# Kernel tuning notes

Hardware: AMD Instinct MI355X
Metric: run time of the kernel (lower is better)

Reference implementation:

```python
import jax, jax.numpy as jnp
import numpy as np

B, N, D = 8, 1024, 1024
E, H = 16, 4096
CAP_FACTOR = 1.25  # training-mode capacity factor
NUM_CLASSES = 345


def setup_inputs() -> dict:
    key = jax.random.key(0)
    k1, k2, k3, k4 = jax.random.split(key, 4)
    inputs = jax.random.normal(k1, (B, N, D), dtype=jnp.float32)
    current_y = jax.random.randint(k2, (B,), 0, NUM_CLASSES, dtype=jnp.int32)
    std1 = 1.0 / np.sqrt(H)  # init_ uses 1/sqrt(last dim)
    std2 = 1.0 / np.sqrt(D)
    w1 = jax.random.uniform(k3, (E, D, H), dtype=jnp.float32, minval=-std1, maxval=std1)
    w2 = jax.random.uniform(k4, (E, H, D), dtype=jnp.float32, minval=-std2, maxval=std2)
    return {"inputs": inputs, "current_y": current_y, "w1": w1, "w2": w2}


def reference(inputs, current_y, w1, w2):
    b, n, d = inputs.shape
    e = w1.shape[0]
    cap = max(min(n, int(n * CAP_FACTOR / e)), 4)  # MIN_EXPERT_CAPACITY=4
    dt = inputs.dtype

    # class-based gating: every token of sample i goes to expert y_i % e
    idx = jnp.broadcast_to(jnp.remainder(current_y, e)[:, None], (b, n))  # (b,n)
    oh = jax.nn.one_hot(idx, e, dtype=dt)                                 # (b,n,e)
    # exclusive cumsum over token dim, masked
    pos = (jnp.cumsum(oh, axis=-2) - oh) * oh                             # (b,n,e)
    mask1 = oh * (pos < cap).astype(dt)                                   # drop overflow tokens
    mask1_flat = mask1.sum(axis=-1)                                       # (b,n)
    pos_flat = pos.sum(axis=-1).astype(jnp.int32)                         # (b,n)

    # combine[b,n,e,c]; out-of-range positions -> zero row (safe_one_hot semantics)
    combine = (mask1_flat[..., None, None]
               * oh[..., None]
               * jax.nn.one_hot(pos_flat, cap, dtype=dt)[..., None, :])
    dispatch = (combine > 0).astype(dt)

    # dispatch tokens to padded expert slots: (e, b, cap, d)
    expert_in = jnp.einsum('bnd,bnec->ebcd', inputs, dispatch).reshape(e, b * cap, d)
    hidden = jax.nn.gelu(jnp.einsum('end,edh->enh', expert_in, w1), approximate=False)
    expert_out = jnp.einsum('enh,ehd->end', hidden, w2).reshape(e, b, cap, d)

    output = jnp.einsum('ebcd,bnec->bnd', expert_out, combine)
    return output
```

## Files before the change

kernel.cpp:

```cpp
#include <hip/hip_runtime.h>
#include <hip/hip_bf16.h>

#define NB   8
#define NTOK 1024
#define DDIM 1024
#define NEXP 16
#define HDIM 4096
#define CAP  80
#define BK   64
#define LDA  (BK + 8)

using bf16x8 = __attribute__((ext_vector_type(8))) __bf16;
using bf16x4 = __attribute__((ext_vector_type(4))) __bf16;
using f32x4  = __attribute__((ext_vector_type(4))) float;

__global__ __launch_bounds__(256) void moe_g1(
    const float* __restrict__ X, const int* __restrict__ Y,
    const float* __restrict__ W1, __bf16* __restrict__ Hid)
{
    const int b     = blockIdx.y;
    const int e     = Y[b] & (NEXP - 1);
    const int nbase = blockIdx.x * 64;
    const int tid   = threadIdx.x;
    const int w     = tid >> 6;
    const int l     = tid & 63;
    const int q     = l >> 4;
    const int r     = l & 15;
    const int n     = nbase + w * 16 + r;
    const int kb    = tid & 15;
    const int hb    = tid >> 4;
    const int arow  = tid >> 4;
    const int akg   = tid & 15;

    __shared__ __bf16 As[2][CAP][LDA];
    __shared__ __bf16 Bt[2][64][LDA];

    const float* Xb  = X  + (size_t)b * NTOK * DDIM;
    const float* W1e = W1 + (size_t)e * DDIM * HDIM;

    f32x4 acc[5];
    #pragma unroll
    for (int i = 0; i < 5; ++i) acc[i] = f32x4{0.f, 0.f, 0.f, 0.f};

    float4 a_reg[5];
    float4 b_reg[4];

    #pragma unroll
    for (int it = 0; it < 5; ++it)
        a_reg[it] = *(const float4*)&Xb[(size_t)(arow + 16 * it) * DDIM + akg * 4];
    #pragma unroll
    for (int kk = 0; kk < 4; ++kk)
        b_reg[kk] = *(const float4*)&W1e[(size_t)(kb * 4 + kk) * HDIM + nbase + hb * 4];

    int cur = 0;
    for (int t = 0; t < DDIM / BK; ++t) {
        #pragma unroll
        for (int it = 0; it < 5; ++it) {
            float4 v = a_reg[it];
            bf16x4 p = {(__bf16)v.x, (__bf16)v.y, (__bf16)v.z, (__bf16)v.w};
            *(bf16x4*)&As[cur][arow + 16 * it][akg * 4] = p;
        }
        {
            bf16x4 p0 = {(__bf16)b_reg[0].x, (__bf16)b_reg[1].x, (__bf16)b_reg[2].x, (__bf16)b_reg[3].x};
            bf16x4 p1 = {(__bf16)b_reg[0].y, (__bf16)b_reg[1].y, (__bf16)b_reg[2].y, (__bf16)b_reg[3].y};
            bf16x4 p2 = {(__bf16)b_reg[0].z, (__bf16)b_reg[1].z, (__bf16)b_reg[2].z, (__bf16)b_reg[3].z};
            bf16x4 p3 = {(__bf16)b_reg[0].w, (__bf16)b_reg[1].w, (__bf16)b_reg[2].w, (__bf16)b_reg[3].w};
            *(bf16x4*)&Bt[cur][hb * 4 + 0][kb * 4] = p0;
            *(bf16x4*)&Bt[cur][hb * 4 + 1][kb * 4] = p1;
            *(bf16x4*)&Bt[cur][hb * 4 + 2][kb * 4] = p2;
            *(bf16x4*)&Bt[cur][hb * 4 + 3][kb * 4] = p3;
        }
        __syncthreads();

        if (t + 1 < DDIM / BK) {
            const int k0 = (t + 1) * BK;
            #pragma unroll
            for (int it = 0; it < 5; ++it)
                a_reg[it] = *(const float4*)&Xb[(size_t)(arow + 16 * it) * DDIM + k0 + akg * 4];
            #pragma unroll
            for (int kk = 0; kk < 4; ++kk)
                b_reg[kk] = *(const float4*)&W1e[(size_t)(k0 + kb * 4 + kk) * HDIM + nbase + hb * 4];
        }

        #pragma unroll
        for (int s = 0; s < 2; ++s) {
            bf16x8 bf = *(const bf16x8*)&Bt[cur][w * 16 + r][s * 32 + q * 8];
            #pragma unroll
            for (int mt = 0; mt < 5; ++mt) {
                bf16x8 af = *(const bf16x8*)&As[cur][mt * 16 + r][s * 32 + q * 8];
                acc[mt] = __builtin_amdgcn_mfma_f32_16x16x32_bf16(af, bf, acc[mt], 0, 0, 0);
            }
        }
        cur ^= 1;
    }

    __bf16* Hb = Hid + (size_t)b * CAP * HDIM;
    #pragma unroll
    for (int mt = 0; mt < 5; ++mt)
        #pragma unroll
        for (int v = 0; v < 4; ++v) {
            int m = mt * 16 + q * 4 + v;
            float x = acc[mt][v];
            float g = 0.5f * x * (1.0f + erff(x * 0.70710678118654752f));
            Hb[(size_t)m * HDIM + n] = (__bf16)g;
        }
}

__global__ __launch_bounds__(256) void moe_g2(
    const __bf16* __restrict__ Hid, const int* __restrict__ Y,
    const float* __restrict__ W2, float* __restrict__ Out)
{
    const int b     = blockIdx.y;
    const int e     = Y[b] & (NEXP - 1);
    const int nbase = blockIdx.x * 64;
    const int kz    = blockIdx.z * (HDIM / 4);
    const int tid   = threadIdx.x;
    const int w     = tid >> 6;
    const int l     = tid & 63;
    const int q     = l >> 4;
    const int r     = l & 15;
    const int n     = nbase + w * 16 + r;
    const int kb    = tid & 15;
    const int hb    = tid >> 4;
    const int arow  = tid >> 4;
    const int akg   = tid & 15;

    __shared__ __bf16 As[2][CAP][LDA];
    __shared__ __bf16 Bt[2][64][LDA];

    const __bf16* Hb  = Hid + (size_t)b * CAP * HDIM;
    const float*  W2e = W2  + (size_t)e * HDIM * DDIM;

    f32x4 acc[5];
    #pragma unroll
    for (int i = 0; i < 5; ++i) acc[i] = f32x4{0.f, 0.f, 0.f, 0.f};

    uint2  a_reg[5];
    float4 b_reg[4];

    #pragma unroll
    for (int it = 0; it < 5; ++it)
        a_reg[it] = *(const uint2*)&Hb[(size_t)(arow + 16 * it) * HDIM + kz + akg * 4];
    #pragma unroll
    for (int kk = 0; kk < 4; ++kk)
        b_reg[kk] = *(const float4*)&W2e[(size_t)(kz + kb * 4 + kk) * DDIM + nbase + hb * 4];

    int cur = 0;
    for (int t = 0; t < (HDIM / 4) / BK; ++t) {
        #pragma unroll
        for (int it = 0; it < 5; ++it)
            *(uint2*)&As[cur][arow + 16 * it][akg * 4] = a_reg[it];
        {
            bf16x4 p0 = {(__bf16)b_reg[0].x, (__bf16)b_reg[1].x, (__bf16)b_reg[2].x, (__bf16)b_reg[3].x};
            bf16x4 p1 = {(__bf16)b_reg[0].y, (__bf16)b_reg[1].y, (__bf16)b_reg[2].y, (__bf16)b_reg[3].y};
            bf16x4 p2 = {(__bf16)b_reg[0].z, (__bf16)b_reg[1].z, (__bf16)b_reg[2].z, (__bf16)b_reg[3].z};
            bf16x4 p3 = {(__bf16)b_reg[0].w, (__bf16)b_reg[1].w, (__bf16)b_reg[2].w, (__bf16)b_reg[3].w};
            *(bf16x4*)&Bt[cur][hb * 4 + 0][kb * 4] = p0;
            *(bf16x4*)&Bt[cur][hb * 4 + 1][kb * 4] = p1;
            *(bf16x4*)&Bt[cur][hb * 4 + 2][kb * 4] = p2;
            *(bf16x4*)&Bt[cur][hb * 4 + 3][kb * 4] = p3;
        }
        __syncthreads();

        if (t + 1 < (HDIM / 4) / BK) {
            const int k0 = kz + (t + 1) * BK;
            #pragma unroll
            for (int it = 0; it < 5; ++it)
                a_reg[it] = *(const uint2*)&Hb[(size_t)(arow + 16 * it) * HDIM + k0 + akg * 4];
            #pragma unroll
            for (int kk = 0; kk < 4; ++kk)
                b_reg[kk] = *(const float4*)&W2e[(size_t)(k0 + kb * 4 + kk) * DDIM + nbase + hb * 4];
        }

        #pragma unroll
        for (int s = 0; s < 2; ++s) {
            bf16x8 bf = *(const bf16x8*)&Bt[cur][w * 16 + r][s * 32 + q * 8];
            #pragma unroll
            for (int mt = 0; mt < 5; ++mt) {
                bf16x8 af = *(const bf16x8*)&As[cur][mt * 16 + r][s * 32 + q * 8];
                acc[mt] = __builtin_amdgcn_mfma_f32_16x16x32_bf16(af, bf, acc[mt], 0, 0, 0);
            }
        }
        cur ^= 1;
    }

    float* Ob = Out + (size_t)b * NTOK * DDIM;
    #pragma unroll
    for (int mt = 0; mt < 5; ++mt)
        #pragma unroll
        for (int v = 0; v < 4; ++v) {
            int m = mt * 16 + q * 4 + v;
            atomicAdd(&Ob[(size_t)m * DDIM + n], acc[mt][v]);
        }
}

extern "C" void kernel_launch(void* const* d_in, const int* in_sizes, int n_in,
                              void* d_out, int out_size, void* d_ws, size_t ws_size,
                              hipStream_t stream) {
    const float* X  = (const float*)d_in[0];
    const int*   Y  = (const int*)d_in[1];
    const float* W1 = (const float*)d_in[2];
    const float* W2 = (const float*)d_in[3];
    float*  Out = (float*)d_out;
    __bf16* Hid = (__bf16*)d_ws;

    hipMemsetAsync(d_out, 0, (size_t)out_size * sizeof(float), stream);

    moe_g1<<<dim3(HDIM / 64, NB), 256, 0, stream>>>(X, Y, W1, Hid);
    moe_g2<<<dim3(DDIM / 64, NB, 4), 256, 0, stream>>>(Hid, Y, W2, Out);
}
```

Measured before the change: 484.3 us.

## Prepack weights and inputs to bf16 MFMA fragment layout before GEMMs

Adds pre-pass kernels that convert the first CAP rows of X to bf16 and repack each used expert's W1/W2 into a bf16 layout matching the MFMA B-fragment order. The GEMM kernels then load fragments straight from global memory, with no LDS staging, no __syncthreads and no in-loop fp32-to-bf16 conversion. The aim is to remove the shared-memory and conversion overhead in the main loops. In exchange it adds extra passes that write and re-read packed weights, and it needs about 272MB of workspace; if the workspace is smaller, the original kernels run instead.

```diff
diff --git a/kernel.cpp b/kernel.cpp
--- a/kernel.cpp
+++ b/kernel.cpp
@@ -14,44 +14,160 @@
 using bf16x4 = __attribute__((ext_vector_type(4))) __bf16;
 using f32x4  = __attribute__((ext_vector_type(4))) float;
 
+__global__ __launch_bounds__(256) void xpre(const float* __restrict__ X,
+                                            __bf16* __restrict__ Xb16)
+{
+    int idx = blockIdx.x * 256 + threadIdx.x;
+    int b   = idx / (CAP * 256);
+    int rem = idx % (CAP * 256);
+    int m   = rem >> 8, c = rem & 255;
+    float4 v = *(const float4*)&X[((size_t)b * NTOK + m) * DDIM + c * 4];
+    bf16x4 p = {(__bf16)v.x, (__bf16)v.y, (__bf16)v.z, (__bf16)v.w};
+    *(bf16x4*)&Xb16[((size_t)b * CAP + m) * DDIM + c * 4] = p;
+}
+
+__global__ __launch_bounds__(512) void wpre(const float* __restrict__ W,
+                                            const int* __restrict__ Y,
+                                            __bf16* __restrict__ P,
+                                            int K, int H, int NB_, int KT_)
+{
+    const int e = blockIdx.z;
+    bool used = false;
+    #pragma unroll
+    for (int i = 0; i < NB; ++i) used |= ((Y[i] & (NEXP - 1)) == e);
+    if (!used) return;
+
+    const int ks  = blockIdx.y;
+    const int hc  = blockIdx.x;
+    const int t   = threadIdx.x;
+    const int q3  = t >> 7;
+    const int h0g = t & 127;
+    const int hg  = hc * 512 + h0g * 4;
+    const int k0  = ks * 32 + q3 * 8;
+
+    const float* Ws = W + (size_t)e * K * H;
+    float4 v[8];
+    #pragma unroll
+    for (int j = 0; j < 8; ++j)
+        v[j] = *(const float4*)&Ws[(size_t)(k0 + j) * H + hg];
+
+    bf16x8 o0, o1, o2, o3;
+    #pragma unroll
+    for (int j = 0; j < 8; ++j) {
+        o0[j] = (__bf16)v[j].x; o1[j] = (__bf16)v[j].y;
+        o2[j] = (__bf16)v[j].z; o3[j] = (__bf16)v[j].w;
+    }
+
+    const int nb = hg >> 6, wv = (hg >> 4) & 3, l0 = q3 * 16 + (hg & 15);
+    __bf16* dst = P + ((((size_t)(e * NB_ + nb) * KT_ + ks) * 4 + wv) * 64 + l0) * 8;
+    *(bf16x8*)&dst[0]  = o0;
+    *(bf16x8*)&dst[8]  = o1;
+    *(bf16x8*)&dst[16] = o2;
+    *(bf16x8*)&dst[24] = o3;
+}
+
 __global__ __launch_bounds__(256) void moe_g1(
+    const __bf16* __restrict__ Xb16, const int* __restrict__ Y,
+    const __bf16* __restrict__ P1, __bf16* __restrict__ Hid)
+{
+    const int b  = blockIdx.y;
+    const int e  = Y[b] & (NEXP - 1);
+    const int tid = threadIdx.x;
+    const int w  = tid >> 6, l = tid & 63, q = l >> 4, r = l & 15;
+    const int n  = blockIdx.x * 64 + w * 16 + r;
+
+    const __bf16* Xb  = Xb16 + (size_t)b * CAP * DDIM;
+    const __bf16* pan = P1 + (size_t)(e * 64 + blockIdx.x) * 32 * 2048
+                           + (size_t)w * 512 + (size_t)l * 8;
+
+    f32x4 acc[5];
+    #pragma unroll
+    for (int i = 0; i < 5; ++i) acc[i] = f32x4{0.f, 0.f, 0.f, 0.f};
+
+    #pragma unroll 4
+    for (int t = 0; t < 32; ++t) {
+        bf16x8 bf = *(const bf16x8*)&pan[(size_t)t * 2048];
+        #pragma unroll
+        for (int mt = 0; mt < 5; ++mt) {
+            bf16x8 af = *(const bf16x8*)&Xb[(size_t)(mt * 16 + r) * DDIM + t * 32 + q * 8];
+            acc[mt] = __builtin_amdgcn_mfma_f32_16x16x32_bf16(af, bf, acc[mt], 0, 0, 0);
+        }
+    }
+
+    __bf16* Hb = Hid + (size_t)b * CAP * HDIM;
+    #pragma unroll
+    for (int mt = 0; mt < 5; ++mt)
+        #pragma unroll
+        for (int v = 0; v < 4; ++v) {
+            int m = mt * 16 + q * 4 + v;
+            float x = acc[mt][v];
+            float g = 0.5f * x * (1.0f + erff(x * 0.70710678118654752f));
+            Hb[(size_t)m * HDIM + n] = (__bf16)g;
+        }
+}
+
+__global__ __launch_bounds__(256) void moe_g2(
+    const __bf16* __restrict__ Hid, const int* __restrict__ Y,
+    const __bf16* __restrict__ P2, float* __restrict__ Out)
+{
+    const int b  = blockIdx.y;
+    const int e  = Y[b] & (NEXP - 1);
+    const int tid = threadIdx.x;
+    const int w  = tid >> 6, l = tid & 63, q = l >> 4, r = l & 15;
+    const int n  = blockIdx.x * 64 + w * 16 + r;
+    const int kz = blockIdx.z * (HDIM / 4);
+
+    const __bf16* Hb  = Hid + (size_t)b * CAP * HDIM;
+    const __bf16* pan = P2 + (size_t)(e * 16 + blockIdx.x) * 128 * 2048
+                           + (size_t)(blockIdx.z * 32) * 2048
+                           + (size_t)w * 512 + (size_t)l * 8;
+
+    f32x4 acc[5];
+    #pragma unroll
+    for (int i = 0; i < 5; ++i) acc[i] = f32x4{0.f, 0.f, 0.f, 0.f};
+
+    #pragma unroll 4
+    for (int t = 0; t < 32; ++t) {
+        bf16x8 bf = *(const bf16x8*)&pan[(size_t)t * 2048];
+        #pragma unroll
+        for (int mt = 0; mt < 5; ++mt) {
+            bf16x8 af = *(const bf16x8*)&Hb[(size_t)(mt * 16 + r) * HDIM + kz + t * 32 + q * 8];
+            acc[mt] = __builtin_amdgcn_mfma_f32_16x16x32_bf16(af, bf, acc[mt], 0, 0, 0);
+        }
+    }
+
+    float* Ob = Out + (size_t)b * NTOK * DDIM;
+    #pragma unroll
+    for (int mt = 0; mt < 5; ++mt)
+        #pragma unroll
+        for (int v = 0; v < 4; ++v) {
+            int m = mt * 16 + q * 4 + v;
+            atomicAdd(&Ob[(size_t)m * DDIM + n], acc[mt][v]);
+        }
+}
+
+__global__ __launch_bounds__(256) void moe_g1_fb(
     const float* __restrict__ X, const int* __restrict__ Y,
     const float* __restrict__ W1, __bf16* __restrict__ Hid)
 {
-    const int b     = blockIdx.y;
-    const int e     = Y[b] & (NEXP - 1);
-    const int nbase = blockIdx.x * 64;
-    const int tid   = threadIdx.x;
-    const int w     = tid >> 6;
-    const int l     = tid & 63;
-    const int q     = l >> 4;
-    const int r     = l & 15;
-    const int n     = nbase + w * 16 + r;
-    const int kb    = tid & 15;
-    const int hb    = tid >> 4;
-    const int arow  = tid >> 4;
-    const int akg   = tid & 15;
-
+    const int b = blockIdx.y, e = Y[b] & (NEXP - 1), nbase = blockIdx.x * 64;
+    const int tid = threadIdx.x, w = tid >> 6, l = tid & 63, q = l >> 4, r = l & 15;
+    const int n = nbase + w * 16 + r;
+    const int kb = tid & 15, hb = tid >> 4, arow = tid >> 4, akg = tid & 15;
     __shared__ __bf16 As[2][CAP][LDA];
     __shared__ __bf16 Bt[2][64][LDA];
-
-    const float* Xb  = X  + (size_t)b * NTOK * DDIM;
+    const float* Xb = X + (size_t)b * NTOK * DDIM;
     const float* W1e = W1 + (size_t)e * DDIM * HDIM;
-
     f32x4 acc[5];
     #pragma unroll
     for (int i = 0; i < 5; ++i) acc[i] = f32x4{0.f, 0.f, 0.f, 0.f};
-
-    float4 a_reg[5];
-    float4 b_reg[4];
-
+    float4 a_reg[5]; float4 b_reg[4];
     #pragma unroll
     for (int it = 0; it < 5; ++it)
         a_reg[it] = *(const float4*)&Xb[(size_t)(arow + 16 * it) * DDIM + akg * 4];
     #pragma unroll
     for (int kk = 0; kk < 4; ++kk)
         b_reg[kk] = *(const float4*)&W1e[(size_t)(kb * 4 + kk) * HDIM + nbase + hb * 4];
-
     int cur = 0;
     for (int t = 0; t < DDIM / BK; ++t) {
         #pragma unroll
@@ -71,7 +187,6 @@
             *(bf16x4*)&Bt[cur][hb * 4 + 3][kb * 4] = p3;
         }
         __syncthreads();
-
         if (t + 1 < DDIM / BK) {
             const int k0 = (t + 1) * BK;
             #pragma unroll
@@ -81,7 +196,6 @@
             for (int kk = 0; kk < 4; ++kk)
                 b_reg[kk] = *(const float4*)&W1e[(size_t)(k0 + kb * 4 + kk) * HDIM + nbase + hb * 4];
         }
-
         #pragma unroll
         for (int s = 0; s < 2; ++s) {
             bf16x8 bf = *(const bf16x8*)&Bt[cur][w * 16 + r][s * 32 + q * 8];
@@ -93,7 +207,6 @@
         }
         cur ^= 1;
     }
-
     __bf16* Hb = Hid + (size_t)b * CAP * HDIM;
     #pragma unroll
     for (int mt = 0; mt < 5; ++mt)
@@ -106,45 +219,29 @@
         }
 }
 
-__global__ __launch_bounds__(256) void moe_g2(
+__global__ __launch_bounds__(256) void moe_g2_fb(
     const __bf16* __restrict__ Hid, const int* __restrict__ Y,
     const float* __restrict__ W2, float* __restrict__ Out)
 {
-    const int b     = blockIdx.y;
-    const int e     = Y[b] & (NEXP - 1);
-    const int nbase = blockIdx.x * 64;
-    const int kz    = blockIdx.z * (HDIM / 4);
-    const int tid   = threadIdx.x;
-    const int w     = tid >> 6;
-    const int l     = tid & 63;
-    const int q     = l >> 4;
-    const int r     = l & 15;
-    const int n     = nbase + w * 16 + r;
-    const int kb    = tid & 15;
-    const int hb    = tid >> 4;
-    const int arow  = tid >> 4;
-    const int akg   = tid & 15;
-
+    const int b = blockIdx.y, e = Y[b] & (NEXP - 1), nbase = blockIdx.x * 64;
+    const int kz = blockIdx.z * (HDIM / 4);
+    const int tid = threadIdx.x, w = tid >> 6, l = tid & 63, q = l >> 4, r = l & 15;
+    const int n = nbase + w * 16 + r;
+    const int kb = tid & 15, hb = tid >> 4, arow = tid >> 4, akg = tid & 15;
     __shared__ __bf16 As[2][CAP][LDA];
     __shared__ __bf16 Bt[2][64][LDA];
-
-    const __bf16* Hb  = Hid + (size_t)b * CAP * HDIM;
-    const float*  W2e = W2  + (size_t)e * HDIM * DDIM;
-
+    const __bf16* Hb = Hid + (size_t)b * CAP * HDIM;
+    const float* W2e = W2 + (size_t)e * HDIM * DDIM;
     f32x4 acc[5];
     #pragma unroll
     for (int i = 0; i < 5; ++i) acc[i] = f32x4{0.f, 0.f, 0.f, 0.f};
-
-    uint2  a_reg[5];
-    float4 b_reg[4];
-
+    uint2 a_reg[5]; float4 b_reg[4];
     #pragma unroll
     for (int it = 0; it < 5; ++it)
         a_reg[it] = *(const uint2*)&Hb[(size_t)(arow + 16 * it) * HDIM + kz + akg * 4];
     #pragma unroll
     for (int kk = 0; kk < 4; ++kk)
         b_reg[kk] = *(const float4*)&W2e[(size_t)(kz + kb * 4 + kk) * DDIM + nbase + hb * 4];
-
     int cur = 0;
     for (int t = 0; t < (HDIM / 4) / BK; ++t) {
         #pragma unroll
@@ -161,7 +258,6 @@
             *(bf16x4*)&Bt[cur][hb * 4 + 3][kb * 4] = p3;
         }
         __syncthreads();
-
         if (t + 1 < (HDIM / 4) / BK) {
             const int k0 = kz + (t + 1) * BK;
             #pragma unroll
@@ -171,7 +267,6 @@
             for (int kk = 0; kk < 4; ++kk)
                 b_reg[kk] = *(const float4*)&W2e[(size_t)(k0 + kb * 4 + kk) * DDIM + nbase + hb * 4];
         }
-
         #pragma unroll
         for (int s = 0; s < 2; ++s) {
             bf16x8 bf = *(const bf16x8*)&Bt[cur][w * 16 + r][s * 32 + q * 8];
@@ -183,7 +278,6 @@
         }
         cur ^= 1;
     }
-
     float* Ob = Out + (size_t)b * NTOK * DDIM;
     #pragma unroll
     for (int mt = 0; mt < 5; ++mt)
@@ -201,11 +295,24 @@
     const int*   Y  = (const int*)d_in[1];
     const float* W1 = (const float*)d_in[2];
     const float* W2 = (const float*)d_in[3];
-    float*  Out = (float*)d_out;
-    __bf16* Hid = (__bf16*)d_ws;
+    float* Out = (float*)d_out;
+
+    uint8_t* ws = (uint8_t*)d_ws;
+    __bf16* Hid  = (__bf16*)ws;
+    __bf16* Xb16 = (__bf16*)(ws + (6u  << 20));
+    __bf16* P1   = (__bf16*)(ws + (16u << 20));
+    __bf16* P2   = (__bf16*)(ws + (144u << 20));
 
     hipMemsetAsync(d_out, 0, (size_t)out_size * sizeof(float), stream);
 
-    moe_g1<<<dim3(HDIM / 64, NB), 256, 0, stream>>>(X, Y, W1, Hid);
-    moe_g2<<<dim3(DDIM / 64, NB, 4), 256, 0, stream>>>(Hid, Y, W2, Out);
-}
+    if (ws_size >= (size_t)(272u << 20)) {
+        xpre<<<dim3(NB * CAP * 256 / 256), 256, 0, stream>>>(X, Xb16);
+        wpre<<<dim3(8, 32, 16),  512, 0, stream>>>(W1, Y, P1, DDIM, HDIM, 64, 32);
+        wpre<<<dim3(2, 128, 16), 512, 0, stream>>>(W2, Y, P2, HDIM, DDIM, 16, 128);
+        moe_g1<<<dim3(HDIM / 64, NB),    256, 0, stream>>>(Xb16, Y, P1, Hid);
+        moe_g2<<<dim3(DDIM / 64, NB, 4), 256, 0, stream>>>(Hid, Y, P2, Out);
+    } else {
+        moe_g1_fb<<<dim3(HDIM / 64, NB),    256, 0, stream>>>(X, Y, W1, Hid);
+        moe_g2_fb<<<dim3(DDIM / 64, NB, 4), 256, 0, stream>>>(Hid, Y, W2, Out);
+    }
+}
```

After: 588.1 us. 1.21x slower.

## Split-K both GEMMs with partial buffers and separate reduce kernels

Applied to the files above, without the earlier changes.

Both expert GEMMs now use 512-thread blocks with 128-wide N tiles and split the K dimension (2-way for the first, 8-way for the second). Partial sums go to fp32 workspace buffers instead of being finished in place. Two new elementwise kernels reduce them: one applies GELU and converts to bf16, the other sums the output partials and writes them directly, replacing the atomicAdd epilogue. The aim is more blocks per GEMM and no atomics, at the cost of extra workspace traffic and two additional launches.

```diff
diff --git a/kernel.cpp b/kernel.cpp
--- a/kernel.cpp
+++ b/kernel.cpp
@@ -8,19 +8,21 @@
 #define HDIM 4096
 #define CAP  80
 #define BK   64
+#define BN   128
 #define LDA  (BK + 8)
 
 using bf16x8 = __attribute__((ext_vector_type(8))) __bf16;
 using bf16x4 = __attribute__((ext_vector_type(4))) __bf16;
 using f32x4  = __attribute__((ext_vector_type(4))) float;
 
-__global__ __launch_bounds__(256) void moe_g1(
+__global__ __launch_bounds__(512) void moe_g1(
     const float* __restrict__ X, const int* __restrict__ Y,
-    const float* __restrict__ W1, __bf16* __restrict__ Hid)
+    const float* __restrict__ W1, float* __restrict__ Hpart)
 {
     const int b     = blockIdx.y;
     const int e     = Y[b] & (NEXP - 1);
-    const int nbase = blockIdx.x * 64;
+    const int nbase = blockIdx.x * BN;
+    const int kz    = blockIdx.z * 512;
     const int tid   = threadIdx.x;
     const int w     = tid >> 6;
     const int l     = tid & 63;
@@ -29,11 +31,9 @@
     const int n     = nbase + w * 16 + r;
     const int kb    = tid & 15;
     const int hb    = tid >> 4;
-    const int arow  = tid >> 4;
-    const int akg   = tid & 15;
 
     __shared__ __bf16 As[2][CAP][LDA];
-    __shared__ __bf16 Bt[2][64][LDA];
+    __shared__ __bf16 Bt[2][BN][LDA];
 
     const float* Xb  = X  + (size_t)b * NTOK * DDIM;
     const float* W1e = W1 + (size_t)e * DDIM * HDIM;
@@ -42,23 +42,32 @@
     #pragma unroll
     for (int i = 0; i < 5; ++i) acc[i] = f32x4{0.f, 0.f, 0.f, 0.f};
 
-    float4 a_reg[5];
+    float4 a_reg[3];
     float4 b_reg[4];
 
     #pragma unroll
-    for (int it = 0; it < 5; ++it)
-        a_reg[it] = *(const float4*)&Xb[(size_t)(arow + 16 * it) * DDIM + akg * 4];
+    for (int it = 0; it < 3; ++it) {
+        int idx = tid + 512 * it;
+        if (it < 2 || idx < CAP * 16) {
+            int row = idx >> 4, kg = idx & 15;
+            a_reg[it] = *(const float4*)&Xb[(size_t)row * DDIM + kz + kg * 4];
+        }
+    }
     #pragma unroll
     for (int kk = 0; kk < 4; ++kk)
-        b_reg[kk] = *(const float4*)&W1e[(size_t)(kb * 4 + kk) * HDIM + nbase + hb * 4];
+        b_reg[kk] = *(const float4*)&W1e[(size_t)(kz + kb * 4 + kk) * HDIM + nbase + hb * 4];
 
     int cur = 0;
-    for (int t = 0; t < DDIM / BK; ++t) {
-        #pragma unroll
-        for (int it = 0; it < 5; ++it) {
-            float4 v = a_reg[it];
-            bf16x4 p = {(__bf16)v.x, (__bf16)v.y, (__bf16)v.z, (__bf16)v.w};
-            *(bf16x4*)&As[cur][arow + 16 * it][akg * 4] = p;
+    for (int t = 0; t < 8; ++t) {
+        #pragma unroll
+        for (int it = 0; it < 3; ++it) {
+            int idx = tid + 512 * it;
+            if (it < 2 || idx < CAP * 16) {
+                int row = idx >> 4, kg = idx & 15;
+                float4 v = a_reg[it];
+                bf16x4 p = {(__bf16)v.x, (__bf16)v.y, (__bf16)v.z, (__bf16)v.w};
+                *(bf16x4*)&As[cur][row][kg * 4] = p;
+            }
         }
         {
             bf16x4 p0 = {(__bf16)b_reg[0].x, (__bf16)b_reg[1].x, (__bf16)b_reg[2].x, (__bf16)b_reg[3].x};
@@ -72,11 +81,16 @@
         }
         __syncthreads();
 
-        if (t + 1 < DDIM / BK) {
-            const int k0 = (t + 1) * BK;
-            #pragma unroll
-            for (int it = 0; it < 5; ++it)
-                a_reg[it] = *(const float4*)&Xb[(size_t)(arow + 16 * it) * DDIM + k0 + akg * 4];
+        if (t + 1 < 8) {
+            const int k0 = kz + (t + 1) * BK;
+            #pragma unroll
+            for (int it = 0; it < 3; ++it) {
+                int idx = tid + 512 * it;
+                if (it < 2 || idx < CAP * 16) {
+                    int row = idx >> 4, kg = idx & 15;
+                    a_reg[it] = *(const float4*)&Xb[(size_t)row * DDIM + k0 + kg * 4];
+                }
+            }
             #pragma unroll
             for (int kk = 0; kk < 4; ++kk)
                 b_reg[kk] = *(const float4*)&W1e[(size_t)(k0 + kb * 4 + kk) * HDIM + nbase + hb * 4];
@@ -94,26 +108,41 @@
         cur ^= 1;
     }
 
-    __bf16* Hb = Hid + (size_t)b * CAP * HDIM;
+    float* Hp = Hpart + ((size_t)blockIdx.z * NB + b) * CAP * HDIM;
     #pragma unroll
     for (int mt = 0; mt < 5; ++mt)
         #pragma unroll
         for (int v = 0; v < 4; ++v) {
             int m = mt * 16 + q * 4 + v;
-            float x = acc[mt][v];
-            float g = 0.5f * x * (1.0f + erff(x * 0.70710678118654752f));
-            Hb[(size_t)m * HDIM + n] = (__bf16)g;
-        }
-}
-
-__global__ __launch_bounds__(256) void moe_g2(
+            Hp[(size_t)m * HDIM + n] = acc[mt][v];
+        }
+}
+
+__global__ __launch_bounds__(256) void gelu_red(const float* __restrict__ Hpart,
+                                                __bf16* __restrict__ Hid)
+{
+    size_t i4 = (size_t)blockIdx.x * 256 + threadIdx.x;
+    const size_t SL = (size_t)NB * CAP * HDIM;
+    float4 v0 = *(const float4*)&Hpart[i4 * 4];
+    float4 v1 = *(const float4*)&Hpart[SL + i4 * 4];
+    float s[4] = {v0.x + v1.x, v0.y + v1.y, v0.z + v1.z, v0.w + v1.w};
+    bf16x4 p;
+    #pragma unroll
+    for (int j = 0; j < 4; ++j) {
+        float x = s[j];
+        p[j] = (__bf16)(0.5f * x * (1.0f + erff(x * 0.70710678118654752f)));
+    }
+    *(bf16x4*)&Hid[i4 * 4] = p;
+}
+
+__global__ __launch_bounds__(512) void moe_g2(
     const __bf16* __restrict__ Hid, const int* __restrict__ Y,
-    const float* __restrict__ W2, float* __restrict__ Out)
+    const float* __restrict__ W2, float* __restrict__ Opart)
 {
     const int b     = blockIdx.y;
     const int e     = Y[b] & (NEXP - 1);
-    const int nbase = blockIdx.x * 64;
-    const int kz    = blockIdx.z * (HDIM / 4);
+    const int nbase = blockIdx.x * BN;
+    const int kz    = blockIdx.z * 512;
     const int tid   = threadIdx.x;
     const int w     = tid >> 6;
     const int l     = tid & 63;
@@ -122,11 +151,9 @@
     const int n     = nbase + w * 16 + r;
     const int kb    = tid & 15;
     const int hb    = tid >> 4;
-    const int arow  = tid >> 4;
-    const int akg   = tid & 15;
 
     __shared__ __bf16 As[2][CAP][LDA];
-    __shared__ __bf16 Bt[2][64][LDA];
+    __shared__ __bf16 Bt[2][BN][LDA];
 
     const __bf16* Hb  = Hid + (size_t)b * CAP * HDIM;
     const float*  W2e = W2  + (size_t)e * HDIM * DDIM;
@@ -135,21 +162,31 @@
     #pragma unroll
     for (int i = 0; i < 5; ++i) acc[i] = f32x4{0.f, 0.f, 0.f, 0.f};
 
-    uint2  a_reg[5];
+    uint2  a_reg[3];
     float4 b_reg[4];
 
     #pragma unroll
-    for (int it = 0; it < 5; ++it)
-        a_reg[it] = *(const uint2*)&Hb[(size_t)(arow + 16 * it) * HDIM + kz + akg * 4];
+    for (int it = 0; it < 3; ++it) {
+        int idx = tid + 512 * it;
+        if (it < 2 || idx < CAP * 16) {
+            int row = idx >> 4, kg = idx & 15;
+            a_reg[it] = *(const uint2*)&Hb[(size_t)row * HDIM + kz + kg * 4];
+        }
+    }
     #pragma unroll
     for (int kk = 0; kk < 4; ++kk)
         b_reg[kk] = *(const float4*)&W2e[(size_t)(kz + kb * 4 + kk) * DDIM + nbase + hb * 4];
 
     int cur = 0;
-    for (int t = 0; t < (HDIM / 4) / BK; ++t) {
-        #pragma unroll
-        for (int it = 0; it < 5; ++it)
-            *(uint2*)&As[cur][arow + 16 * it][akg * 4] = a_reg[it];
+    for (int t = 0; t < 8; ++t) {
+        #pragma unroll
+        for (int it = 0; it < 3; ++it) {
+            int idx = tid + 512 * it;
+            if (it < 2 || idx < CAP * 16) {
+                int row = idx >> 4, kg = idx & 15;
+                *(uint2*)&As[cur][row][kg * 4] = a_reg[it];
+            }
+        }
         {
             bf16x4 p0 = {(__bf16)b_reg[0].x, (__bf16)b_reg[1].x, (__bf16)b_reg[2].x, (__bf16)b_reg[3].x};
             bf16x4 p1 = {(__bf16)b_reg[0].y, (__bf16)b_reg[1].y, (__bf16)b_reg[2].y, (__bf16)b_reg[3].y};
@@ -162,11 +199,16 @@
         }
         __syncthreads();
 
-        if (t + 1 < (HDIM / 4) / BK) {
+        if (t + 1 < 8) {
             const int k0 = kz + (t + 1) * BK;
             #pragma unroll
-            for (int it = 0; it < 5; ++it)
-                a_reg[it] = *(const uint2*)&Hb[(size_t)(arow + 16 * it) * HDIM + k0 + akg * 4];
+            for (int it = 0; it < 3; ++it) {
+                int idx = tid + 512 * it;
+                if (it < 2 || idx < CAP * 16) {
+                    int row = idx >> 4, kg = idx & 15;
+                    a_reg[it] = *(const uint2*)&Hb[(size_t)row * HDIM + k0 + kg * 4];
+                }
+            }
             #pragma unroll
             for (int kk = 0; kk < 4; ++kk)
                 b_reg[kk] = *(const float4*)&W2e[(size_t)(k0 + kb * 4 + kk) * DDIM + nbase + hb * 4];
@@ -184,14 +226,32 @@
         cur ^= 1;
     }
 
-    float* Ob = Out + (size_t)b * NTOK * DDIM;
+    float* Op = Opart + ((size_t)blockIdx.z * NB + b) * CAP * DDIM;
     #pragma unroll
     for (int mt = 0; mt < 5; ++mt)
         #pragma unroll
         for (int v = 0; v < 4; ++v) {
             int m = mt * 16 + q * 4 + v;
-            atomicAdd(&Ob[(size_t)m * DDIM + n], acc[mt][v]);
-        }
+            Op[(size_t)m * DDIM + n] = acc[mt][v];
+        }
+}
+
+__global__ __launch_bounds__(256) void out_red(const float* __restrict__ Opart,
+                                               float* __restrict__ Out)
+{
+    size_t i4 = (size_t)blockIdx.x * 256 + threadIdx.x;
+    const size_t SL = (size_t)NB * CAP * DDIM;
+    float4 s = *(const float4*)&Opart[i4 * 4];
+    #pragma unroll
+    for (int z = 1; z < 8; ++z) {
+        float4 v = *(const float4*)&Opart[(size_t)z * SL + i4 * 4];
+        s.x += v.x; s.y += v.y; s.z += v.z; s.w += v.w;
+    }
+    size_t i = i4 * 4;
+    size_t b = i / ((size_t)CAP * DDIM);
+    size_t rem = i % ((size_t)CAP * DDIM);
+    size_t m = rem / DDIM, d = rem % DDIM;
+    *(float4*)&Out[(b * NTOK + m) * DDIM + d] = s;
 }
 
 extern "C" void kernel_launch(void* const* d_in, const int* in_sizes, int n_in,
@@ -201,11 +261,17 @@
     const int*   Y  = (const int*)d_in[1];
     const float* W1 = (const float*)d_in[2];
     const float* W2 = (const float*)d_in[3];
-    float*  Out = (float*)d_out;
-    __bf16* Hid = (__bf16*)d_ws;
+    float* Out = (float*)d_out;
+
+    uint8_t* ws = (uint8_t*)d_ws;
+    __bf16* Hid   = (__bf16*)ws;
+    float*  Hpart = (float*)(ws + (8u  << 20));
+    float*  Opart = (float*)(ws + (32u << 20));
 
     hipMemsetAsync(d_out, 0, (size_t)out_size * sizeof(float), stream);
 
-    moe_g1<<<dim3(HDIM / 64, NB), 256, 0, stream>>>(X, Y, W1, Hid);
-    moe_g2<<<dim3(DDIM / 64, NB, 4), 256, 0, stream>>>(Hid, Y, W2, Out);
-}
+    moe_g1<<<dim3(HDIM / BN, NB, 2), 512, 0, stream>>>(X, Y, W1, Hpart);
+    gelu_red<<<dim3(NB * CAP * HDIM / 4 / 256), 256, 0, stream>>>(Hpart, Hid);
+    moe_g2<<<dim3(DDIM / BN, NB, 8), 512, 0, stream>>>(Hid, Y, W2, Opart);
+    out_red<<<dim3(NB * CAP * DDIM / 4 / 256), 256, 0, stream>>>(Opart, Out);
+}
```

Measured after the change: 492.0 us. About the same (+1.6%).
